# Optimization experiments

Measured on AMD Instinct MI355X. Metric: run time of the kernel, lower is better.

## Reference

```python
import jax, jax.numpy as jnp
import numpy as np

D_MODEL = 1024
NUM_HEADS = 16
DEPTH = D_MODEL // NUM_HEADS
EPS = 1e-6


def setup_inputs() -> dict:
    key = jax.random.key(0)
    ks = jax.random.split(key, 9)
    B, S = 4, 2048
    scale = 1.0 / np.sqrt(D_MODEL)
    inp = {
        "inputs": jax.random.normal(ks[0], (B, S, D_MODEL), dtype=jnp.float32),
        "Wq": jax.random.normal(ks[1], (D_MODEL, D_MODEL), dtype=jnp.float32) * scale,
        "bq": jnp.zeros((D_MODEL,), dtype=jnp.float32),
        "Wk": jax.random.normal(ks[2], (D_MODEL, D_MODEL), dtype=jnp.float32) * scale,
        "bk": jnp.zeros((D_MODEL,), dtype=jnp.float32),
        "Wv": jax.random.normal(ks[3], (D_MODEL, D_MODEL), dtype=jnp.float32) * scale,
        "bv": jnp.zeros((D_MODEL,), dtype=jnp.float32),
        "Wo": jax.random.normal(ks[4], (D_MODEL, D_MODEL), dtype=jnp.float32) * scale,
        "bo": jnp.zeros((D_MODEL,), dtype=jnp.float32),
        "gamma": jnp.ones((D_MODEL,), dtype=jnp.float32),
        "beta": jnp.zeros((D_MODEL,), dtype=jnp.float32),
    }
    return inp


def _layer_norm(x, gamma, beta):
    mu = jnp.mean(x, axis=-1, keepdims=True)
    var = jnp.mean(jnp.square(x - mu), axis=-1, keepdims=True)
    return (x - mu) * jax.lax.rsqrt(var + EPS) * gamma + beta


def reference(inputs, Wq, bq, Wk, bk, Wv, bv, Wo, bo, gamma, beta):
    B, S, _ = inputs.shape
    # QKV projections, split heads: [B, H, S, depth]
    def split_heads(x):
        return x.reshape(B, S, NUM_HEADS, DEPTH).transpose(0, 2, 1, 3)

    q = split_heads(inputs @ Wq + bq)
    k = split_heads(inputs @ Wk + bk)
    v = split_heads(inputs @ Wv + bv)

    # scores: [B, H, S, S]
    scores = jnp.einsum("bhqd,bhkd->bhqk", q, k) / jnp.sqrt(
        jnp.asarray(DEPTH, dtype=inputs.dtype))
    attn = jax.nn.softmax(scores, axis=-1)  # dropout is identity in eval mode
    out = jnp.einsum("bhqk,bhkd->bhqd", attn, v)
    out = out.transpose(0, 2, 1, 3).reshape(B, S, D_MODEL)
    out = out @ Wo + bo  # dropout2 identity in eval mode
    return _layer_norm(inputs + out, gamma, beta)
```

## Files before the change

### kernel.cpp

```cpp
#include <hip/hip_runtime.h>
#include <hip/hip_bf16.h>


typedef __bf16 bf16;
typedef __bf16 bf16x4 __attribute__((ext_vector_type(4)));
typedef __bf16 bf16x8 __attribute__((ext_vector_type(8)));
typedef float floatx4 __attribute__((ext_vector_type(4)));

#define MFMA16(a, b, c) __builtin_amdgcn_mfma_f32_16x16x32_bf16((a), (b), (c), 0, 0, 0)

static __device__ __forceinline__ floatx4 vmax4(floatx4 a, floatx4 b) {
    floatx4 r;
    r[0] = fmaxf(a[0], b[0]); r[1] = fmaxf(a[1], b[1]);
    r[2] = fmaxf(a[2], b[2]); r[3] = fmaxf(a[3], b[3]);
    return r;
}

__global__ __launch_bounds__(256) void convert_kernel(
    const float* __restrict__ x, bf16* __restrict__ xb)
{
    const int i = blockIdx.x * 256 + threadIdx.x;
    const float4 v = ((const float4*)x)[i];
    bf16x4 r;
    r[0] = (bf16)v.x; r[1] = (bf16)v.y; r[2] = (bf16)v.z; r[3] = (bf16)v.w;
    ((bf16x4*)xb)[i] = r;
}

__global__ __launch_bounds__(256) void transpose_kernel(
    const float* __restrict__ Wq, const float* __restrict__ Wk,
    const float* __restrict__ Wv, const float* __restrict__ Wo,
    bf16* __restrict__ WT, bf16* __restrict__ WoT)
{
    __shared__ float tile[32][33];
    const int z = blockIdx.z;
    const float* src = (z == 0) ? Wq : (z == 1) ? Wk : (z == 2) ? Wv : Wo;
    bf16* dst = (z < 3) ? (WT + (long)z * 1024 * 1024) : WoT;
    const int n0 = blockIdx.x * 32, k0 = blockIdx.y * 32;
    const int tx = threadIdx.x & 31, ty = threadIdx.x >> 5;
#pragma unroll
    for (int i = 0; i < 32; i += 8)
        tile[ty + i][tx] = src[(long)(k0 + ty + i) * 1024 + n0 + tx];
    __syncthreads();
#pragma unroll
    for (int i = 0; i < 32; i += 8)
        dst[(long)(n0 + ty + i) * 1024 + k0 + tx] = (bf16)tile[tx][ty + i];
}

template <int MODE>
__global__ __launch_bounds__(256, 2) void gemm_kernel(
    const bf16* __restrict__ A, const bf16* __restrict__ Bt,
    const float* __restrict__ b0, const float* __restrict__ b1,
    const float* __restrict__ b2, const float* __restrict__ X,
    bf16* __restrict__ Qo, bf16* __restrict__ Ko, bf16* __restrict__ Vto,
    bf16* __restrict__ Tmpb, int N, int K)
{
    constexpr int LDT = 40;
    constexpr int NBX = (MODE == 0) ? 24 : 8;
    constexpr int NWG = NBX * 64;
    constexpr int CPX = NWG / 8;
    __shared__ __align__(16) bf16 As[128 * LDT];
    __shared__ __align__(16) bf16 Bs[128 * LDT];
    const int t = threadIdx.x;
    const int lane = t & 63;
    const int w = t >> 6;
    const int wm = w >> 1, wn = w & 1;
    const int g = lane >> 4, c = lane & 15;

    const int id = blockIdx.y * NBX + blockIdx.x;
    const int swz = (id & 7) * CPX + (id >> 3);
    const int bm = (swz / NBX) * 128;
    const int bn = (swz % NBX) * 128;

    const int srow = t >> 2;
    const int scol = (t & 3) * 8;

    floatx4 acc[4][4];
#pragma unroll
    for (int i = 0; i < 4; ++i)
#pragma unroll
        for (int j = 0; j < 4; ++j) acc[i][j] = floatx4{0.f, 0.f, 0.f, 0.f};

    const bf16* Ap0 = A + (long)(bm + srow) * K + scol;
    const bf16* Ap1 = A + (long)(bm + 64 + srow) * K + scol;
    const bf16* Bp0 = Bt + (long)(bn + srow) * K + scol;
    const bf16* Bp1 = Bt + (long)(bn + 64 + srow) * K + scol;

    uint4 a0 = *(const uint4*)(Ap0);
    uint4 a1 = *(const uint4*)(Ap1);
    uint4 q0 = *(const uint4*)(Bp0);
    uint4 q1 = *(const uint4*)(Bp1);

    for (int k0 = 0; k0 < K; k0 += 32) {
        __syncthreads();
        *(uint4*)&As[srow * LDT + scol] = a0;
        *(uint4*)&As[(64 + srow) * LDT + scol] = a1;
        *(uint4*)&Bs[srow * LDT + scol] = q0;
        *(uint4*)&Bs[(64 + srow) * LDT + scol] = q1;
        __syncthreads();
        if (k0 + 32 < K) {
            a0 = *(const uint4*)(Ap0 + k0 + 32);
            a1 = *(const uint4*)(Ap1 + k0 + 32);
            q0 = *(const uint4*)(Bp0 + k0 + 32);
            q1 = *(const uint4*)(Bp1 + k0 + 32);
        }
        bf16x8 af[4], bfv[4];
#pragma unroll
        for (int i = 0; i < 4; ++i)
            af[i] = *(const bf16x8*)&As[(wm * 64 + i * 16 + c) * LDT + g * 8];
#pragma unroll
        for (int j = 0; j < 4; ++j)
            bfv[j] = *(const bf16x8*)&Bs[(wn * 64 + j * 16 + c) * LDT + g * 8];
#pragma unroll
        for (int i = 0; i < 4; ++i)
#pragma unroll
            for (int j = 0; j < 4; ++j)
                acc[i][j] = MFMA16(af[i], bfv[j], acc[i][j]);
    }

    if (MODE == 0) {
#pragma unroll
        for (int j = 0; j < 4; ++j) {
            const int col = bn + wn * 64 + j * 16 + c;
            const int sec = col >> 10;
            const int nn = col & 1023;
            const int h = nn >> 6, dd = nn & 63;
            const float* bp = (sec == 0) ? b0 : (sec == 1) ? b1 : b2;
            const float bias = bp[nn];
#pragma unroll
            for (int i = 0; i < 4; ++i) {
                const int r0 = bm + wm * 64 + i * 16 + g * 4;
                if (sec == 2) {
                    bf16x4 pack;
#pragma unroll
                    for (int reg = 0; reg < 4; ++reg)
                        pack[reg] = (bf16)(acc[i][j][reg] + bias);
                    const int b_ = r0 >> 11, sr = r0 & 2047;
                    *(bf16x4*)&Vto[((long)(b_ * 16 + h) * 64 + dd) * 2048 + sr] = pack;
                } else {
#pragma unroll
                    for (int reg = 0; reg < 4; ++reg) {
                        const int r = r0 + reg;
                        const int b_ = r >> 11, sr = r & 2047;
                        const float v = acc[i][j][reg] + bias;
                        if (sec == 0)
                            Qo[((long)(b_ * 16 + h) * 2048 + sr) * 64 + dd] =
                                (bf16)(v * 0.18033688011112042f);
                        else
                            Ko[((long)(b_ * 16 + h) * 2048 + sr) * 64 + dd] = (bf16)v;
                    }
                }
            }
        }
    } else {
#pragma unroll
        for (int j = 0; j < 4; ++j) {
            const int col = bn + wn * 64 + j * 16 + c;
            const float bias = b0[col];
#pragma unroll
            for (int i = 0; i < 4; ++i) {
#pragma unroll
                for (int reg = 0; reg < 4; ++reg) {
                    const int r = bm + wm * 64 + i * 16 + g * 4 + reg;
                    Tmpb[(long)r * N + col] =
                        (bf16)(acc[i][j][reg] + bias + X[(long)r * N + col]);
                }
            }
        }
    }
}

__global__ __launch_bounds__(256, 2) void flash_kernel(
    const bf16* __restrict__ Q, const bf16* __restrict__ Kc,
    const bf16* __restrict__ Vt, bf16* __restrict__ O)
{
    constexpr int KSTR = 72;
    constexpr int VSTR = 72;
    constexpr int PSTR = 72;
    __shared__ __align__(16) bf16 Ks[64 * KSTR];
    __shared__ __align__(16) bf16 Vs[64 * VSTR];
    __shared__ __align__(16) bf16 Pl[4 * 32 * PSTR];
    const int t = threadIdx.x;
    const int lane = t & 63;
    const int w = t >> 6;
    const int g = lane >> 4, c = lane & 15;
    const int bh = blockIdx.x;
    const int b_ = bh >> 4, h = bh & 15;
    const bf16* Qp = Q + (long)bh * 2048 * 64;
    const bf16* Kp = Kc + (long)bh * 2048 * 64;
    const bf16* Vp = Vt + (long)bh * 64 * 2048;
    const int q0 = blockIdx.y * 128 + w * 32;
    bf16* Pw = Pl + w * 32 * PSTR;

    bf16x8 qf[2][2];
#pragma unroll
    for (int qs = 0; qs < 2; ++qs)
#pragma unroll
        for (int p = 0; p < 2; ++p)
            qf[qs][p] = *(const bf16x8*)(Qp + (long)(q0 + qs * 16 + c) * 64 + p * 32 + g * 8);

    float m_c[2] = {-1e30f, -1e30f};
    float l_c[2] = {0.f, 0.f};
    floatx4 o[2][4];
#pragma unroll
    for (int qs = 0; qs < 2; ++qs)
#pragma unroll
        for (int dd = 0; dd < 4; ++dd) o[qs][dd] = floatx4{0.f, 0.f, 0.f, 0.f};

    for (int kt = 0; kt < 32; ++kt) {
        __syncthreads();
        {
            uint4 kr[2], vr[2];
#pragma unroll
            for (int i = 0; i < 2; ++i) {
                const int idx = i * 256 + t;
                kr[i] = *(const uint4*)(Kp + (long)kt * 4096 + idx * 8);
                vr[i] = *(const uint4*)(Vp + (long)(idx >> 3) * 2048 + kt * 64 + (idx & 7) * 8);
            }
#pragma unroll
            for (int i = 0; i < 2; ++i) {
                const int idx = i * 256 + t;
                *(uint4*)&Ks[(idx >> 3) * KSTR + (idx & 7) * 8] = kr[i];
                *(uint4*)&Vs[(idx >> 3) * VSTR + (idx & 7) * 8] = vr[i];
            }
        }
        __syncthreads();

        floatx4 s[2][4];
#pragma unroll
        for (int ks = 0; ks < 4; ++ks) {
            bf16x8 kf0 = *(const bf16x8*)&Ks[(ks * 16 + c) * KSTR + g * 8];
            bf16x8 kf1 = *(const bf16x8*)&Ks[(ks * 16 + c) * KSTR + 32 + g * 8];
#pragma unroll
            for (int qs = 0; qs < 2; ++qs) {
                floatx4 z = floatx4{0.f, 0.f, 0.f, 0.f};
                z = MFMA16(kf0, qf[qs][0], z);
                z = MFMA16(kf1, qf[qs][1], z);
                s[qs][ks] = z;
            }
        }

#pragma unroll
        for (int qs = 0; qs < 2; ++qs) {
            floatx4 t0 = vmax4(vmax4(s[qs][0], s[qs][1]), vmax4(s[qs][2], s[qs][3]));
            float mx = fmaxf(fmaxf(t0[0], t0[1]), fmaxf(t0[2], t0[3]));
            mx = fmaxf(mx, __shfl_xor(mx, 16, 64));
            mx = fmaxf(mx, __shfl_xor(mx, 32, 64));
            const float mn = fmaxf(m_c[qs], mx);
            const float al = __builtin_amdgcn_exp2f(m_c[qs] - mn);
            m_c[qs] = mn;
            floatx4 a4 = floatx4{0.f, 0.f, 0.f, 0.f};
#pragma unroll
            for (int ks = 0; ks < 4; ++ks) {
#pragma unroll
                for (int r = 0; r < 4; ++r)
                    s[qs][ks][r] = __builtin_amdgcn_exp2f(s[qs][ks][r] - mn);
                a4 += s[qs][ks];
            }
            float rs = (a4[0] + a4[1]) + (a4[2] + a4[3]);
            rs += __shfl_xor(rs, 16, 64);
            rs += __shfl_xor(rs, 32, 64);
            l_c[qs] = l_c[qs] * al + rs;
#pragma unroll
            for (int dd = 0; dd < 4; ++dd)
#pragma unroll
                for (int r = 0; r < 4; ++r) o[qs][dd][r] *= al;
#pragma unroll
            for (int ks = 0; ks < 4; ++ks) {
                bf16x4 pk;
#pragma unroll
                for (int r = 0; r < 4; ++r) pk[r] = (bf16)s[qs][ks][r];
                *(bf16x4*)&Pw[(qs * 16 + c) * PSTR + ks * 16 + g * 4] = pk;
            }
        }
        asm volatile("s_waitcnt lgkmcnt(0)" ::: "memory");
#pragma unroll
        for (int kk = 0; kk < 2; ++kk) {
            bf16x8 pf0 = *(const bf16x8*)&Pw[(0 + c) * PSTR + kk * 32 + g * 8];
            bf16x8 pf1 = *(const bf16x8*)&Pw[(16 + c) * PSTR + kk * 32 + g * 8];
#pragma unroll
            for (int dd = 0; dd < 4; ++dd) {
                bf16x8 vf = *(const bf16x8*)&Vs[(dd * 16 + c) * VSTR + kk * 32 + g * 8];
                o[0][dd] = MFMA16(vf, pf0, o[0][dd]);
                o[1][dd] = MFMA16(vf, pf1, o[1][dd]);
            }
        }
    }

#pragma unroll
    for (int qs = 0; qs < 2; ++qs) {
        const float linv = 1.0f / l_c[qs];
        const int q = q0 + qs * 16 + c;
#pragma unroll
        for (int dd = 0; dd < 4; ++dd) {
            bf16x4 pk;
#pragma unroll
            for (int r = 0; r < 4; ++r) pk[r] = (bf16)(o[qs][dd][r] * linv);
            *(bf16x4*)&O[((long)b_ * 2048 + q) * 1024 + h * 64 + dd * 16 + g * 4] = pk;
        }
    }
}

__global__ __launch_bounds__(256, 2) void ln_kernel(
    const bf16* __restrict__ Tmp, const float* __restrict__ gamma,
    const float* __restrict__ beta, float* __restrict__ out)
{
    const int row = blockIdx.x;
    const int t = threadIdx.x;
    const int lane = t & 63, w = t >> 6;
    const bf16x4 vb = ((const bf16x4*)(Tmp + (long)row * 1024))[t];
    const float xv[4] = {(float)vb[0], (float)vb[1], (float)vb[2], (float)vb[3]};
    float s = xv[0] + xv[1] + xv[2] + xv[3];
    float ss = xv[0] * xv[0] + xv[1] * xv[1] + xv[2] * xv[2] + xv[3] * xv[3];
#pragma unroll
    for (int off = 1; off < 64; off <<= 1) {
        s += __shfl_xor(s, off, 64);
        ss += __shfl_xor(ss, off, 64);
    }
    __shared__ float sb[4], ssb[4];
    if (lane == 0) { sb[w] = s; ssb[w] = ss; }
    __syncthreads();
    s = sb[0] + sb[1] + sb[2] + sb[3];
    ss = ssb[0] + ssb[1] + ssb[2] + ssb[3];
    const float mu = s * (1.0f / 1024.0f);
    const float var = ss * (1.0f / 1024.0f) - mu * mu;
    const float inv = rsqrtf(var + 1e-6f);
    const float4 gm = ((const float4*)gamma)[t];
    const float4 bt = ((const float4*)beta)[t];
    float4 r;
    r.x = (xv[0] - mu) * inv * gm.x + bt.x;
    r.y = (xv[1] - mu) * inv * gm.y + bt.y;
    r.z = (xv[2] - mu) * inv * gm.z + bt.z;
    r.w = (xv[3] - mu) * inv * gm.w + bt.w;
    ((float4*)(out + (long)row * 1024))[t] = r;
}

extern "C" void kernel_launch(void* const* d_in, const int* in_sizes, int n_in,
                              void* d_out, int out_size, void* d_ws, size_t ws_size,
                              hipStream_t stream)
{
    const float* x     = (const float*)d_in[0];
    const float* Wq    = (const float*)d_in[1];
    const float* bq    = (const float*)d_in[2];
    const float* Wk    = (const float*)d_in[3];
    const float* bk    = (const float*)d_in[4];
    const float* Wv    = (const float*)d_in[5];
    const float* bv    = (const float*)d_in[6];
    const float* Wo    = (const float*)d_in[7];
    const float* bo    = (const float*)d_in[8];
    const float* gamma = (const float*)d_in[9];
    const float* beta  = (const float*)d_in[10];
    float* out = (float*)d_out;

    char* ws = (char*)d_ws;
    bf16* xb   = (bf16*)(ws);
    bf16* WT   = (bf16*)(ws + 16777216);
    bf16* Qb   = (bf16*)(ws + 23068672);
    bf16* Kb   = (bf16*)(ws + 39845888);
    bf16* WoT  = (bf16*)(ws + 56623104);
    bf16* Tmpb = (bf16*)(ws);
    bf16* Vtb  = (bf16*)d_out;
    bf16* Ob   = (bf16*)((char*)d_out + 16777216);

    convert_kernel<<<8192, 256, 0, stream>>>(x, xb);
    transpose_kernel<<<dim3(32, 32, 4), 256, 0, stream>>>(Wq, Wk, Wv, Wo, WT, WoT);
    gemm_kernel<0><<<dim3(24, 64), 256, 0, stream>>>(
        xb, WT, bq, bk, bv, nullptr, Qb, Kb, Vtb, nullptr, 3072, 1024);
    flash_kernel<<<dim3(64, 16), 256, 0, stream>>>(Qb, Kb, Vtb, Ob);
    gemm_kernel<1><<<dim3(8, 64), 256, 0, stream>>>(
        Ob, WoT, bo, nullptr, nullptr, x, nullptr, nullptr, nullptr, Tmpb, 1024, 1024);
    ln_kernel<<<8192, 256, 0, stream>>>(Tmpb, gamma, beta, out);
}
```

Measured before the change: 342.2 us.

## Double-buffer K/V tiles with async global-to-LDS loads and XOR swizzle

Replaces the register-staged K/V tile loads in the flash attention kernel with direct global_load_lds transfers into a double-buffered shared-memory array. The next tile is prefetched while the current one is consumed, and the second barrier per iteration is removed. The padded row stride is replaced by an XOR swizzle of 16-byte chunks to avoid LDS bank conflicts. Shared memory use grows, and correctness relies on the single barrier per iteration also waiting for the outstanding async loads.

New measurement: 345.4 us. About the same (+0.9%).

```diff
diff --git a/kernel.cpp b/kernel.cpp
--- a/kernel.cpp
+++ b/kernel.cpp
@@ -14,6 +14,12 @@
     r[0] = fmaxf(a[0], b[0]); r[1] = fmaxf(a[1], b[1]);
     r[2] = fmaxf(a[2], b[2]); r[3] = fmaxf(a[3], b[3]);
     return r;
+}
+
+static __device__ __forceinline__ void gload16(const bf16* g, bf16* lds_base) {
+    __builtin_amdgcn_global_load_lds(
+        (__attribute__((address_space(1))) void*)(g),
+        (__attribute__((address_space(3))) void*)(lds_base), 16, 0, 0);
 }
 
 __global__ __launch_bounds__(256) void convert_kernel(
@@ -173,11 +179,8 @@
     const bf16* __restrict__ Q, const bf16* __restrict__ Kc,
     const bf16* __restrict__ Vt, bf16* __restrict__ O)
 {
-    constexpr int KSTR = 72;
-    constexpr int VSTR = 72;
     constexpr int PSTR = 72;
-    __shared__ __align__(16) bf16 Ks[64 * KSTR];
-    __shared__ __align__(16) bf16 Vs[64 * VSTR];
+    __shared__ __align__(16) bf16 KVs[2][2][64 * 64];
     __shared__ __align__(16) bf16 Pl[4 * 32 * PSTR];
     const int t = threadIdx.x;
     const int lane = t & 63;
@@ -191,6 +194,19 @@
     const int q0 = blockIdx.y * 128 + w * 32;
     bf16* Pw = Pl + w * 32 * PSTR;
 
+    const bf16* ksrc[2];
+    const bf16* vsrc[2];
+    int ldsoff[2];
+#pragma unroll
+    for (int i = 0; i < 2; ++i) {
+        const int ch = (i * 4 + w) * 64 + lane;
+        const int row = ch >> 3, col = ch & 7;
+        const int sw = col ^ (row & 7);
+        ksrc[i] = Kp + (long)(row * 8 + sw) * 8;
+        vsrc[i] = Vp + (long)row * 2048 + sw * 8;
+        ldsoff[i] = (i * 4 + w) * 512;
+    }
+
     bf16x8 qf[2][2];
 #pragma unroll
     for (int qs = 0; qs < 2; ++qs)
@@ -206,30 +222,31 @@
 #pragma unroll
         for (int dd = 0; dd < 4; ++dd) o[qs][dd] = floatx4{0.f, 0.f, 0.f, 0.f};
 
+#pragma unroll
+    for (int i = 0; i < 2; ++i) {
+        gload16(ksrc[i], &KVs[0][0][ldsoff[i]]);
+        gload16(vsrc[i], &KVs[0][1][ldsoff[i]]);
+    }
+
     for (int kt = 0; kt < 32; ++kt) {
         __syncthreads();
-        {
-            uint4 kr[2], vr[2];
+        const int cur = kt & 1;
+        if (kt + 1 < 32) {
 #pragma unroll
             for (int i = 0; i < 2; ++i) {
-                const int idx = i * 256 + t;
-                kr[i] = *(const uint4*)(Kp + (long)kt * 4096 + idx * 8);
-                vr[i] = *(const uint4*)(Vp + (long)(idx >> 3) * 2048 + kt * 64 + (idx & 7) * 8);
-            }
-#pragma unroll
-            for (int i = 0; i < 2; ++i) {
-                const int idx = i * 256 + t;
-                *(uint4*)&Ks[(idx >> 3) * KSTR + (idx & 7) * 8] = kr[i];
-                *(uint4*)&Vs[(idx >> 3) * VSTR + (idx & 7) * 8] = vr[i];
-            }
-        }
-        __syncthreads();
-
+                gload16(ksrc[i] + (long)(kt + 1) * 4096, &KVs[cur ^ 1][0][ldsoff[i]]);
+                gload16(vsrc[i] + (long)(kt + 1) * 64,   &KVs[cur ^ 1][1][ldsoff[i]]);
+            }
+        }
+        const bf16* KsB = KVs[cur][0];
+        const bf16* VsB = KVs[cur][1];
+
+        const int r7 = c & 7;
         floatx4 s[2][4];
 #pragma unroll
         for (int ks = 0; ks < 4; ++ks) {
-            bf16x8 kf0 = *(const bf16x8*)&Ks[(ks * 16 + c) * KSTR + g * 8];
-            bf16x8 kf1 = *(const bf16x8*)&Ks[(ks * 16 + c) * KSTR + 32 + g * 8];
+            bf16x8 kf0 = *(const bf16x8*)&KsB[(ks * 16 + c) * 64 + ((g ^ r7) << 3)];
+            bf16x8 kf1 = *(const bf16x8*)&KsB[(ks * 16 + c) * 64 + (((g + 4) ^ r7) << 3)];
 #pragma unroll
             for (int qs = 0; qs < 2; ++qs) {
                 floatx4 z = floatx4{0.f, 0.f, 0.f, 0.f};
@@ -279,7 +296,7 @@
             bf16x8 pf1 = *(const bf16x8*)&Pw[(16 + c) * PSTR + kk * 32 + g * 8];
 #pragma unroll
             for (int dd = 0; dd < 4; ++dd) {
-                bf16x8 vf = *(const bf16x8*)&Vs[(dd * 16 + c) * VSTR + kk * 32 + g * 8];
+                bf16x8 vf = *(const bf16x8*)&VsB[(dd * 16 + c) * 64 + (((kk * 4 + g) ^ r7) << 3)];
                 o[0][dd] = MFMA16(vf, pf0, o[0][dd]);
                 o[1][dd] = MFMA16(vf, pf1, o[1][dd]);
             }
```

## Double-buffer GEMM tiles with direct global-to-LDS loads

Applied to the files above, without the earlier changes.

The projection GEMM now loads A and B tiles straight into LDS with global_load_lds, skipping the register staging step. It double-buffers the two LDS tiles so the next K-slice is fetched while MFMAs run on the current one, which removes one barrier per iteration. To fit the DMA layout the LDS row padding is dropped (stride 32), so the fragment reads may now hit bank conflicts. Correctness depends on the DMA writes being waited on before the barrier.

Result: no change. 340.1 us (-0.6%).

```diff
diff --git a/kernel.cpp b/kernel.cpp
--- a/kernel.cpp
+++ b/kernel.cpp
@@ -14,6 +14,12 @@
     r[0] = fmaxf(a[0], b[0]); r[1] = fmaxf(a[1], b[1]);
     r[2] = fmaxf(a[2], b[2]); r[3] = fmaxf(a[3], b[3]);
     return r;
+}
+
+static __device__ __forceinline__ void gload16(const bf16* g, bf16* lds_base) {
+    __builtin_amdgcn_global_load_lds(
+        (__attribute__((address_space(1))) void*)(g),
+        (__attribute__((address_space(3))) void*)(lds_base), 16, 0, 0);
 }
 
 __global__ __launch_bounds__(256) void convert_kernel(
@@ -54,12 +60,12 @@
     bf16* __restrict__ Qo, bf16* __restrict__ Ko, bf16* __restrict__ Vto,
     bf16* __restrict__ Tmpb, int N, int K)
 {
-    constexpr int LDT = 40;
+    constexpr int LDT = 32;
     constexpr int NBX = (MODE == 0) ? 24 : 8;
     constexpr int NWG = NBX * 64;
     constexpr int CPX = NWG / 8;
-    __shared__ __align__(16) bf16 As[128 * LDT];
-    __shared__ __align__(16) bf16 Bs[128 * LDT];
+    __shared__ __align__(16) bf16 As[2][128 * LDT];
+    __shared__ __align__(16) bf16 Bs[2][128 * LDT];
     const int t = threadIdx.x;
     const int lane = t & 63;
     const int w = t >> 6;
@@ -71,8 +77,17 @@
     const int bm = (swz / NBX) * 128;
     const int bn = (swz % NBX) * 128;
 
-    const int srow = t >> 2;
-    const int scol = (t & 3) * 8;
+    const bf16* asrc[2];
+    const bf16* bsrc[2];
+    int ldsoff[2];
+#pragma unroll
+    for (int i = 0; i < 2; ++i) {
+        const int ch = (i * 4 + w) * 64 + lane;
+        const int row = ch >> 2, col = ch & 3;
+        asrc[i] = A + (long)(bm + row) * K + col * 8;
+        bsrc[i] = Bt + (long)(bn + row) * K + col * 8;
+        ldsoff[i] = (i * 4 + w) * 512;
+    }
 
     floatx4 acc[4][4];
 #pragma unroll
@@ -80,41 +95,35 @@
 #pragma unroll
         for (int j = 0; j < 4; ++j) acc[i][j] = floatx4{0.f, 0.f, 0.f, 0.f};
 
-    const bf16* Ap0 = A + (long)(bm + srow) * K + scol;
-    const bf16* Ap1 = A + (long)(bm + 64 + srow) * K + scol;
-    const bf16* Bp0 = Bt + (long)(bn + srow) * K + scol;
-    const bf16* Bp1 = Bt + (long)(bn + 64 + srow) * K + scol;
-
-    uint4 a0 = *(const uint4*)(Ap0);
-    uint4 a1 = *(const uint4*)(Ap1);
-    uint4 q0 = *(const uint4*)(Bp0);
-    uint4 q1 = *(const uint4*)(Bp1);
-
+#pragma unroll
+    for (int i = 0; i < 2; ++i) {
+        gload16(asrc[i], &As[0][ldsoff[i]]);
+        gload16(bsrc[i], &Bs[0][ldsoff[i]]);
+    }
+
+    int cur = 0;
     for (int k0 = 0; k0 < K; k0 += 32) {
         __syncthreads();
-        *(uint4*)&As[srow * LDT + scol] = a0;
-        *(uint4*)&As[(64 + srow) * LDT + scol] = a1;
-        *(uint4*)&Bs[srow * LDT + scol] = q0;
-        *(uint4*)&Bs[(64 + srow) * LDT + scol] = q1;
-        __syncthreads();
         if (k0 + 32 < K) {
-            a0 = *(const uint4*)(Ap0 + k0 + 32);
-            a1 = *(const uint4*)(Ap1 + k0 + 32);
-            q0 = *(const uint4*)(Bp0 + k0 + 32);
-            q1 = *(const uint4*)(Bp1 + k0 + 32);
+#pragma unroll
+            for (int i = 0; i < 2; ++i) {
+                gload16(asrc[i] + k0 + 32, &As[cur ^ 1][ldsoff[i]]);
+                gload16(bsrc[i] + k0 + 32, &Bs[cur ^ 1][ldsoff[i]]);
+            }
         }
         bf16x8 af[4], bfv[4];
 #pragma unroll
         for (int i = 0; i < 4; ++i)
-            af[i] = *(const bf16x8*)&As[(wm * 64 + i * 16 + c) * LDT + g * 8];
+            af[i] = *(const bf16x8*)&As[cur][(wm * 64 + i * 16 + c) * LDT + g * 8];
 #pragma unroll
         for (int j = 0; j < 4; ++j)
-            bfv[j] = *(const bf16x8*)&Bs[(wn * 64 + j * 16 + c) * LDT + g * 8];
+            bfv[j] = *(const bf16x8*)&Bs[cur][(wn * 64 + j * 16 + c) * LDT + g * 8];
 #pragma unroll
         for (int i = 0; i < 4; ++i)
 #pragma unroll
             for (int j = 0; j < 4; ++j)
                 acc[i][j] = MFMA16(af[i], bfv[j], acc[i][j]);
+        cur ^= 1;
     }
 
     if (MODE == 0) {
```
